# Kernel tuning notes

Measured on AMD Instinct MI355X. Metric: run time of the kernel, lower is better.

Reference implementation:

```python
import jax, jax.numpy as jnp
import numpy as np

T, D = 1024, 1024            # tokens, model dim
E, K = 16, 4                 # routed experts, top-k
G, TG = 4, 2                 # expert groups, limited (top) groups
INTER = 512                  # moe_inter_dim
SHARED_INTER = 2 * INTER     # n_shared_experts * moe_inter_dim
ROUTE_SCALE = 2.5
STD = 0.02


def setup_inputs() -> dict:
    key = jax.random.key(0)
    ks = jax.random.split(key, 9)
    return {
        "x": jax.random.normal(ks[0], (T, D), jnp.float32),
        "token_mask": jnp.ones((T,), jnp.bool_),
        "gate_w": jax.random.normal(ks[1], (E, D), jnp.float32) * STD,
        "gate_bias": jnp.zeros((E,), jnp.float32),  # e_score_correction_bias (zero-init)
        "gate_projs": jax.random.normal(ks[2], (E, INTER, D), jnp.float32) * STD,
        "up_projs": jax.random.normal(ks[3], (E, INTER, D), jnp.float32) * STD,
        "down_projs": jax.random.normal(ks[4], (E, D, INTER), jnp.float32) * STD,
        "shared_gate": jax.random.normal(ks[5], (SHARED_INTER, D), jnp.float32) * STD,
        "shared_up": jax.random.normal(ks[6], (SHARED_INTER, D), jnp.float32) * STD,
        "shared_down": jax.random.normal(ks[7], (D, SHARED_INTER), jnp.float32) * STD,
    }


def _route(x, gate_w, gate_bias):
    # sigmoid scoring with e_score_correction_bias + group-limited top-k (DeepSeek-V3 style)
    scores = jax.nn.sigmoid(x @ gate_w.T)                      # [T, E]
    s = (scores + gate_bias).reshape(T, G, E // G)             # bias-corrected, grouped
    group_scores = jax.lax.top_k(s, 2)[0].sum(-1)              # [T, G] sum of top-2 per group
    gidx = jax.lax.top_k(group_scores, TG)[1]                  # [T, TG]
    gmask = jax.nn.one_hot(gidx, G, dtype=s.dtype).sum(1)      # [T, G] selected-group mask
    masked = (s * gmask[:, :, None]).reshape(T, E)
    idx = jax.lax.top_k(masked, K)[1]                          # [T, K] expert indices
    w = jnp.take_along_axis(scores, idx, axis=1)               # gather original (unbiased) scores
    w = w / w.sum(-1, keepdims=True) * ROUTE_SCALE             # sigmoid renorm + route scale
    return w.astype(x.dtype), idx


def reference(x, token_mask, gate_w, gate_bias, gate_projs, up_projs,
              down_projs, shared_gate, shared_up, shared_down):
    w, idx = _route(x, gate_w, gate_bias)
    # dense combine weights [T, E]: combine[t, e] = sum_k w[t, k] * (idx[t, k] == e)
    combine = (jax.nn.one_hot(idx, E, dtype=x.dtype) * w[..., None]).sum(1)

    def body(acc, p):
        gp, up, dp, c = p                                      # per-expert SwiGLU
        inter = jax.nn.silu(x @ gp.T) * (x @ up.T)             # [T, INTER]
        return acc + c[:, None] * (inter @ dp.T), None

    routed, _ = jax.lax.scan(
        body, jnp.zeros_like(x), (gate_projs, up_projs, down_projs, combine.T))
    shared = (jax.nn.silu(x @ shared_gate.T) * (x @ shared_up.T)) @ shared_down.T
    return routed + shared
```

## Files before the change

kernel.cpp:

```cpp
#include <hip/hip_runtime.h>
#include <stdint.h>

#define TTOK 1024
#define DMODEL 1024
#define NEXP 16
#define TOPK 4
#define INTER 512
#define NSHI 1024
#define RSCALE 2.5f

typedef __bf16 bf16;
typedef __bf16 bf16x8 __attribute__((ext_vector_type(8)));
typedef __bf16 bf16x4 __attribute__((ext_vector_type(4)));
typedef float f32x4 __attribute__((ext_vector_type(4)));

#define APLANE 2064
#define BPLANE 1040

__global__ __launch_bounds__(256)
void scores_kernel(const float* __restrict__ x, const float* __restrict__ gw,
                   float* __restrict__ scores, bf16* __restrict__ xbf) {
  __shared__ float gws[16 * 1024];
  const int tid = threadIdx.x;
  const float4* gw4 = (const float4*)gw;
#pragma unroll
  for (int i0 = 0; i0 < 4096; i0 += 256) {
    const int i = i0 + tid;
    const int e = i >> 8;
    const int dq = (i & 255) << 2;
    const int dd = (dq + 4 * e) & 1023;
    ((float4*)gws)[(e << 8) + (dd >> 2)] = gw4[i];
  }
  {
    const long xb = (long)blockIdx.x * 1024;
#pragma unroll
    for (int p = 0; p < 4; ++p) {
      const long j = xb + p * 256 + tid;
      const float4 v = ((const float4*)x)[j];
      bf16x4 o;
      o.x = (bf16)v.x; o.y = (bf16)v.y; o.z = (bf16)v.z; o.w = (bf16)v.w;
      ((bf16x4*)xbf)[j] = o;
    }
  }
  __syncthreads();
  const int kq = tid >> 6;
  const int lane = tid & 63;
  const int tl = lane >> 4;
  const int e = lane & 15;
  const long token = (long)blockIdx.x * 4 + tl;
  float acc = 0.f;
  const int dbase = kq * 256;
#pragma unroll 8
  for (int i = 0; i < 256; i += 4) {
    const int d = dbase + i;
    const float4 xv = *(const float4*)&x[token * DMODEL + d];
    const float4 wv = *(const float4*)&gws[(e << 10) + ((d + 4 * e) & 1023)];
    acc += xv.x * wv.x + xv.y * wv.y + xv.z * wv.z + xv.w * wv.w;
  }
  __syncthreads();
  gws[kq * 64 + lane] = acc;
  __syncthreads();
  if (kq == 0) {
    const float s = gws[lane] + gws[64 + lane] + gws[128 + lane] + gws[192 + lane];
    scores[token * 16 + e] = s;
  }
}

__global__ __launch_bounds__(256)
void topk_kernel(const float* __restrict__ scores, const float* __restrict__ gb,
                 int* __restrict__ tokIdx, float* __restrict__ tokW,
                 int* __restrict__ counts) {
  __shared__ int h[NEXP];
  const int tid = threadIdx.x;
  if (tid < NEXP) h[tid] = 0;
  __syncthreads();
  const int t = blockIdx.x * 256 + tid;
  float sc[NEXP], s[NEXP];
#pragma unroll
  for (int e = 0; e < NEXP; ++e) {
    const float l = scores[t * NEXP + e];
    sc[e] = 1.f / (1.f + expf(-l));
    s[e] = sc[e] + gb[e];
  }
  float gsc[4];
#pragma unroll
  for (int g = 0; g < 4; ++g) {
    const float a = s[4 * g], b = s[4 * g + 1], c = s[4 * g + 2], d = s[4 * g + 3];
    gsc[g] = fmaxf(fmaxf(fmaxf(a + b, a + c), fmaxf(a + d, b + c)),
                   fmaxf(b + d, c + d));
  }
  int g0 = 0;
  for (int g = 1; g < 4; ++g) if (gsc[g] > gsc[g0]) g0 = g;
  int g1 = (g0 == 0) ? 1 : 0;
  for (int g = 0; g < 4; ++g) if (g != g0 && gsc[g] > gsc[g1]) g1 = g;
  float m[NEXP];
#pragma unroll
  for (int e = 0; e < NEXP; ++e) {
    const int g = e >> 2;
    m[e] = (g == g0 || g == g1) ? s[e] : -1.f;
  }
  int idx[TOPK]; float wv[TOPK]; float wsum = 0.f;
  for (int k = 0; k < TOPK; ++k) {
    int am = 0; float best = m[0];
    for (int e2 = 1; e2 < NEXP; ++e2)
      if (m[e2] > best) { best = m[e2]; am = e2; }
    idx[k] = am; wv[k] = sc[am]; wsum += sc[am]; m[am] = -2.f;
  }
  const float scl = RSCALE / wsum;
  for (int k = 0; k < TOPK; ++k) {
    tokIdx[t * TOPK + k] = idx[k];
    tokW[t * TOPK + k] = wv[k] * scl;
    atomicAdd(&h[idx[k]], 1);
  }
  __syncthreads();
  if (tid < NEXP) atomicAdd(&counts[tid], h[tid]);
}

__global__ void plan_kernel(const int* __restrict__ counts, int* __restrict__ offs,
                            int* __restrict__ cursors, int* __restrict__ tileE,
                            int* __restrict__ tileR, int* __restrict__ tileCnt) {
  if (threadIdx.x == 0) {
    int acc = 0;
    for (int e = 0; e < NEXP; ++e) { offs[e] = acc; cursors[e] = acc; acc += counts[e]; }
    offs[NEXP] = acc;
    int tc = 0;
    for (int e = 0; e < NEXP; ++e)
      for (int r = offs[e]; r < offs[e + 1]; r += 128) { tileE[tc] = e; tileR[tc] = r; ++tc; }
    for (int r = 0; r < TTOK; r += 128) { tileE[tc] = NEXP; tileR[tc] = r; ++tc; }
    tileCnt[0] = tc;
  }
}

__global__ __launch_bounds__(256)
void fill_kernel(const int* __restrict__ tokIdx, int* __restrict__ cursors,
                 int* __restrict__ slotTok, int* __restrict__ tokSlot) {
  __shared__ int h[NEXP], base[NEXP];
  const int tid = threadIdx.x;
  if (tid < NEXP) h[tid] = 0;
  __syncthreads();
  const int t = blockIdx.x * 256 + tid;
  int myE[TOPK], myR[TOPK];
#pragma unroll
  for (int k = 0; k < TOPK; ++k) {
    myE[k] = tokIdx[t * TOPK + k];
    myR[k] = atomicAdd(&h[myE[k]], 1);
  }
  __syncthreads();
  if (tid < NEXP) base[tid] = atomicAdd(&cursors[tid], h[tid]);
  __syncthreads();
#pragma unroll
  for (int k = 0; k < TOPK; ++k) {
    const int slot = base[myE[k]] + myR[k];
    slotTok[slot] = t;
    tokSlot[t * TOPK + k] = slot;
  }
}

__global__ __launch_bounds__(256, 2)
void gateup_gemm(const bf16* __restrict__ xbf, const int* __restrict__ slotTok,
                 const int* __restrict__ offs, const int* __restrict__ tileE,
                 const int* __restrict__ tileR, const int* __restrict__ tileCnt,
                 const float* __restrict__ Wg, const float* __restrict__ Wu,
                 const float* __restrict__ Sg, const float* __restrict__ Su,
                 bf16* __restrict__ interR, bf16* __restrict__ interS) {
  const int y = blockIdx.y;
  if (y >= tileCnt[0]) return;
  const int e = tileE[y];
  const bool shd = (e == NEXP);
  const int n0 = blockIdx.x * 64;
  if (!shd && n0 >= INTER) return;
  const int rowStart = tileR[y];
  const int rowEnd = shd ? rowStart + 128 : offs[e + 1];
  const float* wgp = shd ? Sg : Wg + (long)e * INTER * DMODEL;
  const float* wup = shd ? Su : Wu + (long)e * INTER * DMODEL;

  __shared__ __attribute__((aligned(16))) char As[8 * APLANE];
  __shared__ __attribute__((aligned(16))) char Bg[8 * BPLANE];
  __shared__ __attribute__((aligned(16))) char Bu[8 * BPLANE];
  __shared__ int tokS[128];

  const int tid = threadIdx.x;
  if (tid < 128) {
    const int r = rowStart + tid;
    tokS[tid] = shd ? r : slotTok[r < rowEnd ? r : rowStart];
  }
  __syncthreads();

  const int arw = tid >> 3;
  const int aoct = tid & 7;
  const bf16* aSrc[4];
#pragma unroll
  for (int p = 0; p < 4; ++p)
    aSrc[p] = xbf + (long)tokS[p * 32 + arw] * DMODEL + aoct * 8;

  const int bu_ = tid >> 7;
  const int u = tid & 127;
  const int brw = u >> 4;
  const int bf4 = u & 15;
  const int boct = bf4 >> 1;
  const int bhalf = bf4 & 1;
  const float* bSrc = (bu_ ? wup : wgp) + (long)n0 * DMODEL + bf4 * 4;
  char* bDst = bu_ ? Bu : Bg;

  const int lane = tid & 63;
  const int wv = tid >> 6;
  const int q = lane >> 4;
  const int l15 = lane & 15;
  const int wm = (wv >> 1) * 64;
  const int wn = (wv & 1) * 32;

  const f32x4 fz = {0.f, 0.f, 0.f, 0.f};
  f32x4 accG[4][2], accU[4][2];
#pragma unroll
  for (int i = 0; i < 4; ++i)
#pragma unroll
    for (int j = 0; j < 2; ++j) { accG[i][j] = fz; accU[i][j] = fz; }

  bf16x8 av[4];
  float4 bv[8];
#pragma unroll
  for (int p = 0; p < 4; ++p) av[p] = *(const bf16x8*)(aSrc[p]);
#pragma unroll
  for (int p = 0; p < 8; ++p)
    bv[p] = *(const float4*)(bSrc + (long)(p * 8 + brw) * DMODEL);

  for (int k0 = 0; k0 < DMODEL; k0 += 64) {
    __syncthreads();
#pragma unroll
    for (int p = 0; p < 4; ++p)
      *(bf16x8*)(As + aoct * APLANE + (p * 32 + arw) * 16) = av[p];
#pragma unroll
    for (int p = 0; p < 8; ++p) {
      bf16x4 w;
      w.x = (bf16)bv[p].x; w.y = (bf16)bv[p].y; w.z = (bf16)bv[p].z; w.w = (bf16)bv[p].w;
      *(bf16x4*)(bDst + boct * BPLANE + (p * 8 + brw) * 16 + bhalf * 8) = w;
    }
    const int kn = k0 + 64;
    if (kn < DMODEL) {
#pragma unroll
      for (int p = 0; p < 4; ++p) av[p] = *(const bf16x8*)(aSrc[p] + kn);
#pragma unroll
      for (int p = 0; p < 8; ++p)
        bv[p] = *(const float4*)(bSrc + (long)(p * 8 + brw) * DMODEL + kn);
    }
    __syncthreads();
#pragma unroll
    for (int kb = 0; kb < 2; ++kb) {
      bf16x8 aF[4];
#pragma unroll
      for (int mi = 0; mi < 4; ++mi)
        aF[mi] = *(const bf16x8*)(As + (4 * kb + q) * APLANE + (wm + 16 * mi + l15) * 16);
#pragma unroll
      for (int ni = 0; ni < 2; ++ni) {
        const int br = wn + 16 * ni + l15;
        const bf16x8 gF = *(const bf16x8*)(Bg + (4 * kb + q) * BPLANE + br * 16);
        const bf16x8 uF = *(const bf16x8*)(Bu + (4 * kb + q) * BPLANE + br * 16);
#pragma unroll
        for (int mi = 0; mi < 4; ++mi) {
          accG[mi][ni] = __builtin_amdgcn_mfma_f32_16x16x32_bf16(aF[mi], gF, accG[mi][ni], 0, 0, 0);
          accU[mi][ni] = __builtin_amdgcn_mfma_f32_16x16x32_bf16(aF[mi], uF, accU[mi][ni], 0, 0, 0);
        }
      }
    }
  }

  bf16* outI = shd ? interS : interR;
  const int ldI = shd ? NSHI : INTER;
#pragma unroll
  for (int mi = 0; mi < 4; ++mi)
#pragma unroll
    for (int r = 0; r < 4; ++r) {
      const int rowLoc = wm + 16 * mi + q * 4 + r;
      const int row = rowStart + rowLoc;
      if (row < rowEnd) {
#pragma unroll
        for (int ni = 0; ni < 2; ++ni) {
          const float gg = accG[mi][ni][r];
          const float uu = accU[mi][ni][r];
          const float sv = gg / (1.f + __expf(-gg)) * uu;
          outI[(long)row * ldI + (n0 + wn + 16 * ni + l15)] = (bf16)sv;
        }
      }
    }
}

__global__ __launch_bounds__(256, 2)
void down_gemm(const bf16* __restrict__ interR, const bf16* __restrict__ interS,
               const int* __restrict__ offs, const int* __restrict__ tileE,
               const int* __restrict__ tileR, const int* __restrict__ tileCnt,
               const float* __restrict__ Wd, const float* __restrict__ Sd,
               float* __restrict__ dsR, float* __restrict__ dsS) {
  const int y = blockIdx.y;
  if (y >= tileCnt[0]) return;
  const int e = tileE[y];
  const bool shd = (e == NEXP);
  const int n0 = blockIdx.x * 64;
  const int rowStart = tileR[y];
  const int rowEnd = shd ? rowStart + 128 : offs[e + 1];
  const int Kd = shd ? NSHI : INTER;
  const bf16* A = shd ? interS : interR;
  const float* wd = shd ? Sd : Wd + (long)e * DMODEL * INTER;

  __shared__ __attribute__((aligned(16))) char As[8 * APLANE];
  __shared__ __attribute__((aligned(16))) char Bs[8 * BPLANE];

  const int tid = threadIdx.x;
  const int arw = tid >> 3;
  const int aoct = tid & 7;
  const bf16* aSrc[4];
#pragma unroll
  for (int p = 0; p < 4; ++p)
    aSrc[p] = A + (long)(rowStart + p * 32 + arw) * Kd + aoct * 8;

  const int brw = tid >> 4;
  const int bf4 = tid & 15;
  const int boct = bf4 >> 1;
  const int bhalf = bf4 & 1;
  const float* bSrc = wd + (long)n0 * Kd + bf4 * 4;

  const int lane = tid & 63;
  const int wv = tid >> 6;
  const int q = lane >> 4;
  const int l15 = lane & 15;
  const int wm = (wv >> 1) * 64;
  const int wn = (wv & 1) * 32;

  const f32x4 fz = {0.f, 0.f, 0.f, 0.f};
  f32x4 acc[4][2];
#pragma unroll
  for (int i = 0; i < 4; ++i)
#pragma unroll
    for (int j = 0; j < 2; ++j) acc[i][j] = fz;

  bf16x8 av[4];
  float4 bv[4];
#pragma unroll
  for (int p = 0; p < 4; ++p) av[p] = *(const bf16x8*)(aSrc[p]);
#pragma unroll
  for (int p = 0; p < 4; ++p)
    bv[p] = *(const float4*)(bSrc + (long)(p * 16 + brw) * Kd);

  for (int k0 = 0; k0 < Kd; k0 += 64) {
    __syncthreads();
#pragma unroll
    for (int p = 0; p < 4; ++p)
      *(bf16x8*)(As + aoct * APLANE + (p * 32 + arw) * 16) = av[p];
#pragma unroll
    for (int p = 0; p < 4; ++p) {
      bf16x4 w;
      w.x = (bf16)bv[p].x; w.y = (bf16)bv[p].y; w.z = (bf16)bv[p].z; w.w = (bf16)bv[p].w;
      *(bf16x4*)(Bs + boct * BPLANE + (p * 16 + brw) * 16 + bhalf * 8) = w;
    }
    const int kn = k0 + 64;
    if (kn < Kd) {
#pragma unroll
      for (int p = 0; p < 4; ++p) av[p] = *(const bf16x8*)(aSrc[p] + kn);
#pragma unroll
      for (int p = 0; p < 4; ++p)
        bv[p] = *(const float4*)(bSrc + (long)(p * 16 + brw) * Kd + kn);
    }
    __syncthreads();
#pragma unroll
    for (int kb = 0; kb < 2; ++kb) {
      bf16x8 aF[4];
#pragma unroll
      for (int mi = 0; mi < 4; ++mi)
        aF[mi] = *(const bf16x8*)(As + (4 * kb + q) * APLANE + (wm + 16 * mi + l15) * 16);
#pragma unroll
      for (int ni = 0; ni < 2; ++ni) {
        const bf16x8 bF = *(const bf16x8*)(Bs + (4 * kb + q) * BPLANE + (wn + 16 * ni + l15) * 16);
#pragma unroll
        for (int mi = 0; mi < 4; ++mi)
          acc[mi][ni] = __builtin_amdgcn_mfma_f32_16x16x32_bf16(aF[mi], bF, acc[mi][ni], 0, 0, 0);
      }
    }
  }

  float* dst = shd ? dsS : dsR;
#pragma unroll
  for (int mi = 0; mi < 4; ++mi)
#pragma unroll
    for (int r = 0; r < 4; ++r) {
      const int rowLoc = wm + 16 * mi + q * 4 + r;
      const int row = rowStart + rowLoc;
      if (row < rowEnd) {
#pragma unroll
        for (int ni = 0; ni < 2; ++ni)
          dst[(long)row * DMODEL + (n0 + wn + 16 * ni + l15)] = acc[mi][ni][r];
      }
    }
}

__global__ __launch_bounds__(256)
void combine_kernel(const float* __restrict__ dsR, const float* __restrict__ dsS,
                    const int* __restrict__ tokSlot, const float* __restrict__ tokW,
                    float* __restrict__ out) {
  const int t = blockIdx.x;
  const int j = threadIdx.x;
  float4 v = ((const float4*)(dsS + (long)t * DMODEL))[j];
#pragma unroll
  for (int k = 0; k < TOPK; ++k) {
    const int s = tokSlot[t * TOPK + k];
    const float w = tokW[t * TOPK + k];
    const float4 r = ((const float4*)(dsR + (long)s * DMODEL))[j];
    v.x += w * r.x; v.y += w * r.y; v.z += w * r.z; v.w += w * r.w;
  }
  ((float4*)(out + (long)t * DMODEL))[j] = v;
}

extern "C" void kernel_launch(void* const* d_in, const int* in_sizes, int n_in,
                              void* d_out, int out_size, void* d_ws, size_t ws_size,
                              hipStream_t stream) {
  const float* x  = (const float*)d_in[0];
  const float* gw = (const float*)d_in[2];
  const float* gb = (const float*)d_in[3];
  const float* gp = (const float*)d_in[4];
  const float* up = (const float*)d_in[5];
  const float* dp = (const float*)d_in[6];
  const float* sg = (const float*)d_in[7];
  const float* su = (const float*)d_in[8];
  const float* sd = (const float*)d_in[9];
  float* out = (float*)d_out;

  char* base = (char*)d_ws;
  size_t off = 0;
  auto alloc = [&](size_t bytes) -> char* {
    off = (off + 255) & ~(size_t)255;
    char* p = base + off;
    off += bytes;
    return p;
  };
  bf16* xbf = (bf16*)alloc((size_t)TTOK * DMODEL * 2);
  bf16* interR = (bf16*)alloc((size_t)(TTOK * TOPK + 128) * INTER * 2);
  bf16* interS = (bf16*)alloc((size_t)TTOK * NSHI * 2);
  float* dsR = (float*)alloc((size_t)TTOK * TOPK * DMODEL * 4);
  float* dsS = (float*)alloc((size_t)TTOK * DMODEL * 4);
  float* scores = (float*)alloc((size_t)TTOK * NEXP * 4);
  int* tokIdx = (int*)alloc(TTOK * TOPK * 4);
  float* tokW = (float*)alloc(TTOK * TOPK * 4);
  int* slotTok = (int*)alloc(TTOK * TOPK * 4);
  int* tokSlot = (int*)alloc(TTOK * TOPK * 4);
  int* counts = (int*)alloc(NEXP * 4);
  int* offs = (int*)alloc((NEXP + 1) * 4);
  int* cursors = (int*)alloc(NEXP * 4);
  int* tileE = (int*)alloc(72 * 4);
  int* tileR = (int*)alloc(72 * 4);
  int* tileCnt = (int*)alloc(4);

  hipMemsetAsync(counts, 0, NEXP * 4, stream);

  scores_kernel<<<TTOK / 4, 256, 0, stream>>>(x, gw, scores, xbf);
  topk_kernel<<<TTOK / 256, 256, 0, stream>>>(scores, gb, tokIdx, tokW, counts);
  plan_kernel<<<1, 64, 0, stream>>>(counts, offs, cursors, tileE, tileR, tileCnt);
  fill_kernel<<<TTOK / 256, 256, 0, stream>>>(tokIdx, cursors, slotTok, tokSlot);

  gateup_gemm<<<dim3(16, 56, 1), 256, 0, stream>>>(
      xbf, slotTok, offs, tileE, tileR, tileCnt, gp, up, sg, su, interR, interS);
  down_gemm<<<dim3(16, 56, 1), 256, 0, stream>>>(
      interR, interS, offs, tileE, tileR, tileCnt, dp, sd, dsR, dsS);
  combine_kernel<<<TTOK, 256, 0, stream>>>(dsR, dsS, tokSlot, tokW, out);
}
```

Baseline: 220.7 us.

## Pre-convert all expert weights to bf16 in one pass before GEMMs

Adds a conversion kernel that casts every routed and shared weight tensor from fp32 to bf16 into a workspace buffer each call. The gate/up and down GEMMs then load bf16x8 weight vectors directly, halving the bytes per tile load and dropping the per-tile in-kernel conversion. The barriers are also replaced with an lgkmcnt wait plus s_barrier. The tradeoff is an extra full pass that reads all weights in fp32 and writes a bf16 copy, and in the GEMMs each weight tile is re-read by several token tiles, so the net effect depends on that reuse.

```diff
diff --git a/kernel.cpp b/kernel.cpp
--- a/kernel.cpp
+++ b/kernel.cpp
@@ -16,6 +16,40 @@
 
 #define APLANE 2064
 #define BPLANE 1040
+
+#define OFF_GP 0L
+#define OFF_UP 8388608L
+#define OFF_DP 16777216L
+#define OFF_SG 25165824L
+#define OFF_SU 26214400L
+#define OFF_SD 27262976L
+#define WTOT   28311552L
+
+#define LGKM_BAR()                                            \
+  do {                                                        \
+    asm volatile("s_waitcnt lgkmcnt(0)" ::: "memory");        \
+    __builtin_amdgcn_s_barrier();                             \
+  } while (0)
+
+__global__ __launch_bounds__(256)
+void convert_kernel(const float* __restrict__ s0, const float* __restrict__ s1,
+                    const float* __restrict__ s2, const float* __restrict__ s3,
+                    const float* __restrict__ s4, const float* __restrict__ s5,
+                    bf16* __restrict__ dst) {
+  const long i = (long)blockIdx.x * 256 + threadIdx.x;
+  const float* src;
+  long local;
+  if (i < 2097152)      { src = s0; local = i; }
+  else if (i < 4194304) { src = s1; local = i - 2097152; }
+  else if (i < 6291456) { src = s2; local = i - 4194304; }
+  else if (i < 6553600) { src = s3; local = i - 6291456; }
+  else if (i < 6815744) { src = s4; local = i - 6553600; }
+  else                  { src = s5; local = i - 6815744; }
+  const float4 v = ((const float4*)src)[local];
+  bf16x4 o;
+  o.x = (bf16)v.x; o.y = (bf16)v.y; o.z = (bf16)v.z; o.w = (bf16)v.w;
+  ((bf16x4*)dst)[i] = o;
+}
 
 __global__ __launch_bounds__(256)
 void scores_kernel(const float* __restrict__ x, const float* __restrict__ gw,
@@ -160,8 +194,7 @@
 void gateup_gemm(const bf16* __restrict__ xbf, const int* __restrict__ slotTok,
                  const int* __restrict__ offs, const int* __restrict__ tileE,
                  const int* __restrict__ tileR, const int* __restrict__ tileCnt,
-                 const float* __restrict__ Wg, const float* __restrict__ Wu,
-                 const float* __restrict__ Sg, const float* __restrict__ Su,
+                 const bf16* __restrict__ wbf,
                  bf16* __restrict__ interR, bf16* __restrict__ interS) {
   const int y = blockIdx.y;
   if (y >= tileCnt[0]) return;
@@ -171,8 +204,8 @@
   if (!shd && n0 >= INTER) return;
   const int rowStart = tileR[y];
   const int rowEnd = shd ? rowStart + 128 : offs[e + 1];
-  const float* wgp = shd ? Sg : Wg + (long)e * INTER * DMODEL;
-  const float* wup = shd ? Su : Wu + (long)e * INTER * DMODEL;
+  const bf16* wgp = shd ? wbf + OFF_SG : wbf + OFF_GP + (long)e * INTER * DMODEL;
+  const bf16* wup = shd ? wbf + OFF_SU : wbf + OFF_UP + (long)e * INTER * DMODEL;
 
   __shared__ __attribute__((aligned(16))) char As[8 * APLANE];
   __shared__ __attribute__((aligned(16))) char Bg[8 * BPLANE];
@@ -195,11 +228,9 @@
 
   const int bu_ = tid >> 7;
   const int u = tid & 127;
-  const int brw = u >> 4;
-  const int bf4 = u & 15;
-  const int boct = bf4 >> 1;
-  const int bhalf = bf4 & 1;
-  const float* bSrc = (bu_ ? wup : wgp) + (long)n0 * DMODEL + bf4 * 4;
+  const int brw = u >> 3;
+  const int boct = u & 7;
+  const bf16* bSrc = (bu_ ? wup : wgp) + (long)(n0 + brw) * DMODEL + boct * 8;
   char* bDst = bu_ ? Bu : Bg;
 
   const int lane = tid & 63;
@@ -217,33 +248,30 @@
     for (int j = 0; j < 2; ++j) { accG[i][j] = fz; accU[i][j] = fz; }
 
   bf16x8 av[4];
-  float4 bv[8];
+  bf16x8 bv[4];
 #pragma unroll
   for (int p = 0; p < 4; ++p) av[p] = *(const bf16x8*)(aSrc[p]);
 #pragma unroll
-  for (int p = 0; p < 8; ++p)
-    bv[p] = *(const float4*)(bSrc + (long)(p * 8 + brw) * DMODEL);
+  for (int p = 0; p < 4; ++p)
+    bv[p] = *(const bf16x8*)(bSrc + (long)(p * 16) * DMODEL);
 
   for (int k0 = 0; k0 < DMODEL; k0 += 64) {
-    __syncthreads();
+    LGKM_BAR();
 #pragma unroll
     for (int p = 0; p < 4; ++p)
       *(bf16x8*)(As + aoct * APLANE + (p * 32 + arw) * 16) = av[p];
 #pragma unroll
-    for (int p = 0; p < 8; ++p) {
-      bf16x4 w;
-      w.x = (bf16)bv[p].x; w.y = (bf16)bv[p].y; w.z = (bf16)bv[p].z; w.w = (bf16)bv[p].w;
-      *(bf16x4*)(bDst + boct * BPLANE + (p * 8 + brw) * 16 + bhalf * 8) = w;
-    }
+    for (int p = 0; p < 4; ++p)
+      *(bf16x8*)(bDst + boct * BPLANE + (p * 16 + brw) * 16) = bv[p];
     const int kn = k0 + 64;
     if (kn < DMODEL) {
 #pragma unroll
       for (int p = 0; p < 4; ++p) av[p] = *(const bf16x8*)(aSrc[p] + kn);
 #pragma unroll
-      for (int p = 0; p < 8; ++p)
-        bv[p] = *(const float4*)(bSrc + (long)(p * 8 + brw) * DMODEL + kn);
-    }
-    __syncthreads();
+      for (int p = 0; p < 4; ++p)
+        bv[p] = *(const bf16x8*)(bSrc + (long)(p * 16) * DMODEL + kn);
+    }
+    LGKM_BAR();
 #pragma unroll
     for (int kb = 0; kb < 2; ++kb) {
       bf16x8 aF[4];
@@ -288,7 +316,7 @@
 void down_gemm(const bf16* __restrict__ interR, const bf16* __restrict__ interS,
                const int* __restrict__ offs, const int* __restrict__ tileE,
                const int* __restrict__ tileR, const int* __restrict__ tileCnt,
-               const float* __restrict__ Wd, const float* __restrict__ Sd,
+               const bf16* __restrict__ wbf,
                float* __restrict__ dsR, float* __restrict__ dsS) {
   const int y = blockIdx.y;
   if (y >= tileCnt[0]) return;
@@ -299,7 +327,7 @@
   const int rowEnd = shd ? rowStart + 128 : offs[e + 1];
   const int Kd = shd ? NSHI : INTER;
   const bf16* A = shd ? interS : interR;
-  const float* wd = shd ? Sd : Wd + (long)e * DMODEL * INTER;
+  const bf16* wd = shd ? wbf + OFF_SD : wbf + OFF_DP + (long)e * DMODEL * INTER;
 
   __shared__ __attribute__((aligned(16))) char As[8 * APLANE];
   __shared__ __attribute__((aligned(16))) char Bs[8 * BPLANE];
@@ -312,11 +340,9 @@
   for (int p = 0; p < 4; ++p)
     aSrc[p] = A + (long)(rowStart + p * 32 + arw) * Kd + aoct * 8;
 
-  const int brw = tid >> 4;
-  const int bf4 = tid & 15;
-  const int boct = bf4 >> 1;
-  const int bhalf = bf4 & 1;
-  const float* bSrc = wd + (long)n0 * Kd + bf4 * 4;
+  const int brw = tid >> 3;
+  const int boct = tid & 7;
+  const bf16* bSrc = wd + (long)(n0 + brw) * Kd + boct * 8;
 
   const int lane = tid & 63;
   const int wv = tid >> 6;
@@ -333,33 +359,30 @@
     for (int j = 0; j < 2; ++j) acc[i][j] = fz;
 
   bf16x8 av[4];
-  float4 bv[4];
+  bf16x8 bv[2];
 #pragma unroll
   for (int p = 0; p < 4; ++p) av[p] = *(const bf16x8*)(aSrc[p]);
 #pragma unroll
-  for (int p = 0; p < 4; ++p)
-    bv[p] = *(const float4*)(bSrc + (long)(p * 16 + brw) * Kd);
+  for (int p = 0; p < 2; ++p)
+    bv[p] = *(const bf16x8*)(bSrc + (long)(p * 32) * Kd);
 
   for (int k0 = 0; k0 < Kd; k0 += 64) {
-    __syncthreads();
+    LGKM_BAR();
 #pragma unroll
     for (int p = 0; p < 4; ++p)
       *(bf16x8*)(As + aoct * APLANE + (p * 32 + arw) * 16) = av[p];
 #pragma unroll
-    for (int p = 0; p < 4; ++p) {
-      bf16x4 w;
-      w.x = (bf16)bv[p].x; w.y = (bf16)bv[p].y; w.z = (bf16)bv[p].z; w.w = (bf16)bv[p].w;
-      *(bf16x4*)(Bs + boct * BPLANE + (p * 16 + brw) * 16 + bhalf * 8) = w;
-    }
+    for (int p = 0; p < 2; ++p)
+      *(bf16x8*)(Bs + boct * BPLANE + (p * 32 + brw) * 16) = bv[p];
     const int kn = k0 + 64;
     if (kn < Kd) {
 #pragma unroll
       for (int p = 0; p < 4; ++p) av[p] = *(const bf16x8*)(aSrc[p] + kn);
 #pragma unroll
-      for (int p = 0; p < 4; ++p)
-        bv[p] = *(const float4*)(bSrc + (long)(p * 16 + brw) * Kd + kn);
-    }
-    __syncthreads();
+      for (int p = 0; p < 2; ++p)
+        bv[p] = *(const bf16x8*)(bSrc + (long)(p * 32) * Kd + kn);
+    }
+    LGKM_BAR();
 #pragma unroll
     for (int kb = 0; kb < 2; ++kb) {
       bf16x8 aF[4];
@@ -430,6 +453,7 @@
     off += bytes;
     return p;
   };
+  bf16* wbf = (bf16*)alloc((size_t)WTOT * 2);
   bf16* xbf = (bf16*)alloc((size_t)TTOK * DMODEL * 2);
   bf16* interR = (bf16*)alloc((size_t)(TTOK * TOPK + 128) * INTER * 2);
   bf16* interS = (bf16*)alloc((size_t)TTOK * NSHI * 2);
@@ -449,14 +473,15 @@
 
   hipMemsetAsync(counts, 0, NEXP * 4, stream);
 
+  convert_kernel<<<27648, 256, 0, stream>>>(gp, up, dp, sg, su, sd, wbf);
   scores_kernel<<<TTOK / 4, 256, 0, stream>>>(x, gw, scores, xbf);
   topk_kernel<<<TTOK / 256, 256, 0, stream>>>(scores, gb, tokIdx, tokW, counts);
   plan_kernel<<<1, 64, 0, stream>>>(counts, offs, cursors, tileE, tileR, tileCnt);
   fill_kernel<<<TTOK / 256, 256, 0, stream>>>(tokIdx, cursors, slotTok, tokSlot);
 
   gateup_gemm<<<dim3(16, 56, 1), 256, 0, stream>>>(
-      xbf, slotTok, offs, tileE, tileR, tileCnt, gp, up, sg, su, interR, interS);
+      xbf, slotTok, offs, tileE, tileR, tileCnt, wbf, interR, interS);
   down_gemm<<<dim3(16, 56, 1), 256, 0, stream>>>(
-      interR, interS, offs, tileE, tileR, tileCnt, dp, sd, dsR, dsS);
+      interR, interS, offs, tileE, tileR, tileCnt, wbf, dsR, dsS);
   combine_kernel<<<TTOK, 256, 0, stream>>>(dsR, dsS, tokSlot, tokW, out);
 }
```

New measurement: 222.8 us. Within noise of the previous version (+0.9%).
